# Kernel optimization log

Hardware: AMD Instinct MI355X
Metric: run time of the kernel (lower is better)

The kernel has to match this reference:

```python
import jax, jax.numpy as jnp
import numpy as np

N_NODES = 50000
N_EDGES = 800000
IN_CH = 128
DIM = 128
OUT_CH = 2
NUM_GRAPHS = 128
BN_EPS = 1e-5


def _linear_params(key, fan_in, fan_out):
    k1, k2 = jax.random.split(key)
    bound = 1.0 / np.sqrt(fan_in)
    w = jax.random.uniform(k1, (fan_in, fan_out), jnp.float32, -bound, bound)
    b = jax.random.uniform(k2, (fan_out,), jnp.float32, -bound, bound)
    return w, b


def setup_inputs() -> dict:
    key = jax.random.key(0)
    ks = jax.random.split(key, 10)
    x = jax.random.normal(ks[0], (N_NODES, IN_CH), jnp.float32)
    edge_index = jax.random.randint(ks[1], (2, N_EDGES), 0, N_NODES, jnp.int64)
    batch = jnp.sort(jax.random.randint(ks[2], (N_NODES,), 0, NUM_GRAPHS, jnp.int64))
    w1_1, b1_1 = _linear_params(ks[3], IN_CH, DIM)
    w1_2, b1_2 = _linear_params(ks[4], DIM, DIM)
    w2_1, b2_1 = _linear_params(ks[5], DIM, DIM)
    w2_2, b2_2 = _linear_params(ks[6], DIM, DIM)
    lin1_w, lin1_b = _linear_params(ks[7], DIM, DIM)
    lin2_w, lin2_b = _linear_params(ks[8], DIM, OUT_CH)
    bnk = jax.random.split(ks[9], 2)
    return {
        'x': x, 'edge_index': edge_index, 'batch': batch,
        'w1_1': w1_1, 'b1_1': b1_1,
        'bn1_g': jax.random.normal(bnk[0], (DIM,), jnp.float32) * 0.1 + 1.0,
        'bn1_b': jnp.zeros((DIM,), jnp.float32),
        'bn1_m': jnp.zeros((DIM,), jnp.float32),
        'bn1_v': jnp.ones((DIM,), jnp.float32),
        'w1_2': w1_2, 'b1_2': b1_2,
        'w2_1': w2_1, 'b2_1': b2_1,
        'bn2_g': jax.random.normal(bnk[1], (DIM,), jnp.float32) * 0.1 + 1.0,
        'bn2_b': jnp.zeros((DIM,), jnp.float32),
        'bn2_m': jnp.zeros((DIM,), jnp.float32),
        'bn2_v': jnp.ones((DIM,), jnp.float32),
        'w2_2': w2_2, 'b2_2': b2_2,
        'lin1_w': lin1_w, 'lin1_b': lin1_b,
        'lin2_w': lin2_w, 'lin2_b': lin2_b,
    }


def _bn_eval(h, g, b, m, v):
    return (h - m) * jax.lax.rsqrt(v + BN_EPS) * g + b


def _gin_conv(x, src, dst, w_a, b_a, bn_g, bn_b, bn_m, bn_v, w_b, b_b):
    # GINConv, eps=0: h = MLP(x + sum_{j->i} x_j)
    agg = jax.ops.segment_sum(x[src], dst, num_segments=x.shape[0])
    h = x + agg
    h = jax.nn.relu(_bn_eval(h @ w_a + b_a, bn_g, bn_b, bn_m, bn_v))
    return jax.nn.relu(h @ w_b + b_b)


def reference(x, edge_index, batch,
              w1_1, b1_1, bn1_g, bn1_b, bn1_m, bn1_v, w1_2, b1_2,
              w2_1, b2_1, bn2_g, bn2_b, bn2_m, bn2_v, w2_2, b2_2,
              lin1_w, lin1_b, lin2_w, lin2_b):
    src, dst = edge_index[0], edge_index[1]
    h = _gin_conv(x, src, dst, w1_1, b1_1, bn1_g, bn1_b, bn1_m, bn1_v, w1_2, b1_2)
    h = _gin_conv(h, src, dst, w2_1, b2_1, bn2_g, bn2_b, bn2_m, bn2_v, w2_2, b2_2)
    # global_add_pool over graph ids
    g = jax.ops.segment_sum(h, batch, num_segments=NUM_GRAPHS)
    g = jax.nn.relu(g @ lin1_w + lin1_b)
    # dropout is identity in eval mode
    return g @ lin2_w + lin2_b
```

## Files before the change

kernel.cpp:

```cpp
#include <hip/hip_runtime.h>
#include <hip/hip_bf16.h>

#define N_NODES 50000
#define N_EDGES 800000
#define DIM 128
#define NUM_GRAPHS 128
#define BN_EPS 1e-5f

constexpr int BK     = 7;
constexpr int NBUCK  = (N_NODES + 127) >> BK;
constexpr int TILE   = 4096;
constexpr int NTILE  = (N_EDGES + TILE - 1) / TILE;
constexpr int CAP    = 4096;
constexpr int NPAD   = N_NODES;

constexpr int XGRID  = 6250;
constexpr int WGRID  = 256;

typedef __attribute__((ext_vector_type(8))) short short8;
typedef __attribute__((ext_vector_type(4))) float f32x4;

__device__ __forceinline__ unsigned short f2bu(float v)
{
    __hip_bfloat16 h = __float2bfloat16(v);
    unsigned short u;
    __builtin_memcpy(&u, &h, 2);
    return u;
}
__device__ __forceinline__ float lo2f(unsigned int v)
{
    return __builtin_bit_cast(float, v << 16);
}
__device__ __forceinline__ float hi2f(unsigned int v)
{
    return __builtin_bit_cast(float, v & 0xffff0000u);
}
__device__ __forceinline__ float b2f(unsigned short u)
{
    return __builtin_bit_cast(float, ((unsigned int)u) << 16);
}

__global__ __launch_bounds__(256)
void setup_kernel(const float* __restrict__ x, __hip_bfloat16* __restrict__ xb,
                  const float* __restrict__ w0, const float* __restrict__ w1,
                  const float* __restrict__ w2, const float* __restrict__ w3,
                  __hip_bfloat16* __restrict__ wt, int* __restrict__ bcur,
                  float* __restrict__ G, __hip_bfloat16* __restrict__ Hb)
{
    int b = blockIdx.x;
    int t = threadIdx.x;
    if (b < XGRID) {
        size_t i = ((size_t)b * 256 + t) * 4;
        float4 v = *reinterpret_cast<const float4*>(x + i);
        uint2 o;
        o.x = (unsigned int)f2bu(v.x) | ((unsigned int)f2bu(v.y) << 16);
        o.y = (unsigned int)f2bu(v.z) | ((unsigned int)f2bu(v.w) << 16);
        *reinterpret_cast<uint2*>(reinterpret_cast<unsigned short*>(xb) + i) = o;
    } else if (b < XGRID + WGRID) {
        int o = (b - XGRID) * 256 + t;
        int m = o >> 14, idx = o & 16383;
        const float* W = (m == 0) ? w0 : (m == 1) ? w1 : (m == 2) ? w2 : w3;
        int n = idx >> 7, k = idx & 127;
        wt[o] = __float2bfloat16(W[k * 128 + n]);
    } else {
        for (int i = t; i < NBUCK; i += 256) bcur[i] = 0;
        for (int i = t; i < NUM_GRAPHS * DIM; i += 256) G[i] = 0.f;
        if (t < 128) {
            xb[(size_t)NPAD * DIM + t] = __float2bfloat16(0.f);
            Hb[(size_t)NPAD * DIM + t] = __float2bfloat16(0.f);
        }
    }
}

__global__ __launch_bounds__(512)
void bscatter_kernel(const int* __restrict__ src, const int* __restrict__ dst,
                     int* __restrict__ bcur, unsigned int* __restrict__ bedge)
{
    __shared__ int h[512];
    __shared__ int s[512];
    __shared__ int lofs[512];
    __shared__ int cur[512];
    __shared__ int gofs[512];
    __shared__ unsigned int stage[TILE];

    int t = threadIdx.x;
    h[t] = 0;
    __syncthreads();

    int e0 = blockIdx.x * TILE;
    for (int i = t; i < TILE; i += 512) {
        int e = e0 + i;
        if (e < N_EDGES) atomicAdd(&h[dst[e] >> BK], 1);
    }
    __syncthreads();

    int v = h[t];
    s[t] = v;
    __syncthreads();
    for (int o = 1; o < 512; o <<= 1) {
        int a = (t >= o) ? s[t - o] : 0;
        __syncthreads();
        s[t] += a;
        __syncthreads();
    }
    int excl = s[t] - v;
    lofs[t] = excl;
    cur[t]  = excl;
    if (t < NBUCK)
        gofs[t] = v ? atomicAdd(&bcur[t], v) : 0;
    __syncthreads();

    const int mtot = s[511];

    for (int i = t; i < TILE; i += 512) {
        int e = e0 + i;
        if (e < N_EDGES) {
            int d = dst[e];
            int b = d >> BK;
            int r = atomicAdd(&cur[b], 1);
            stage[r] = (unsigned int)src[e]
                     | ((unsigned int)(d & 127) << 16)
                     | ((unsigned int)b << 23);
        }
    }
    __syncthreads();

    for (int i = t; i < mtot; i += 512) {
        unsigned int w = stage[i];
        int b = (int)(w >> 23);
        int pos = gofs[b] + (i - lofs[b]);
        if (pos < CAP)
            bedge[(size_t)b * CAP + pos] = w & 0x7fffffu;
    }
}

__global__ __launch_bounds__(256)
void bcsr_kernel(const unsigned int* __restrict__ bedge,
                 const int* __restrict__ bcur,
                 int* __restrict__ rowbeg, int* __restrict__ rowend,
                 unsigned short* __restrict__ elist)
{
    __shared__ int h2[128];
    __shared__ int sc[128];
    __shared__ int cur[128];

    int b  = blockIdx.x;
    int t  = threadIdx.x;
    int m  = bcur[b];
    if (m > CAP) m = CAP;
    const int e0 = b * CAP;
    const unsigned int* be = bedge + (size_t)e0;

    if (t < 128) h2[t] = 0;
    __syncthreads();
    for (int i = t; i < m; i += 256)
        atomicAdd(&h2[(be[i] >> 16) & 127], 1);
    __syncthreads();

    int pc = 0;
    if (t < 128) {
        pc = (h2[t] + 15) & ~15;
        sc[t] = pc;
    }
    __syncthreads();
    for (int o = 1; o < 128; o <<= 1) {
        int a = 0;
        if (t < 128 && t >= o) a = sc[t - o];
        __syncthreads();
        if (t < 128) sc[t] += a;
        __syncthreads();
    }
    if (t < 128) {
        int ex = sc[t] - pc;
        int node = (b << BK) + t;
        if (node < N_NODES) {
            rowbeg[node] = e0 + ex;
            rowend[node] = e0 + ex + pc;
        }
        cur[t] = ex;
        int cnt = h2[t];
        for (int i = ex + cnt; i < ex + pc && i < CAP; ++i)
            elist[e0 + i] = (unsigned short)NPAD;
    }
    __syncthreads();

    for (int i = t; i < m; i += 256) {
        unsigned int w = be[i];
        int n = (int)((w >> 16) & 127);
        int r = atomicAdd(&cur[n], 1);
        if (r < CAP)
            elist[e0 + r] = (unsigned short)(w & 0xffffu);
    }
}

__device__ __forceinline__ void accum8(float* acc, uint4 v)
{
    acc[0] += lo2f(v.x); acc[1] += hi2f(v.x);
    acc[2] += lo2f(v.y); acc[3] += hi2f(v.y);
    acc[4] += lo2f(v.z); acc[5] += hi2f(v.z);
    acc[6] += lo2f(v.w); acc[7] += hi2f(v.w);
}

__global__ __launch_bounds__(256)
void gather_agg_kernel(const __hip_bfloat16* __restrict__ feat,
                       const int* __restrict__ rowbeg,
                       const int* __restrict__ rowend,
                       const unsigned short* __restrict__ elist,
                       __hip_bfloat16* __restrict__ out)
{
    const int node = blockIdx.x * 4 + (threadIdx.x >> 6);
    const int l = threadIdx.x & 63;
    const int g = l & 15;
    const int s = l >> 4;
    const uint4* F = reinterpret_cast<const uint4*>(feat);

    int p = rowbeg[node];
    const int e = rowend[node];

    float acc[8] = {};
    if (s == 0)
        accum8(acc, F[(size_t)node * 16 + g]);

    for (; p + 32 <= e; p += 32) {
        int i0 = elist[p + s];
        int i1 = elist[p + 4 + s];
        int i2 = elist[p + 8 + s];
        int i3 = elist[p + 12 + s];
        int i4 = elist[p + 16 + s];
        int i5 = elist[p + 20 + s];
        int i6 = elist[p + 24 + s];
        int i7 = elist[p + 28 + s];
        uint4 v0 = F[(size_t)i0 * 16 + g];
        uint4 v1 = F[(size_t)i1 * 16 + g];
        uint4 v2 = F[(size_t)i2 * 16 + g];
        uint4 v3 = F[(size_t)i3 * 16 + g];
        uint4 v4 = F[(size_t)i4 * 16 + g];
        uint4 v5 = F[(size_t)i5 * 16 + g];
        uint4 v6 = F[(size_t)i6 * 16 + g];
        uint4 v7 = F[(size_t)i7 * 16 + g];
        accum8(acc, v0);
        accum8(acc, v1);
        accum8(acc, v2);
        accum8(acc, v3);
        accum8(acc, v4);
        accum8(acc, v5);
        accum8(acc, v6);
        accum8(acc, v7);
    }
    if (p < e) {
        int i0 = elist[p + s];
        int i1 = elist[p + 4 + s];
        int i2 = elist[p + 8 + s];
        int i3 = elist[p + 12 + s];
        uint4 v0 = F[(size_t)i0 * 16 + g];
        uint4 v1 = F[(size_t)i1 * 16 + g];
        uint4 v2 = F[(size_t)i2 * 16 + g];
        uint4 v3 = F[(size_t)i3 * 16 + g];
        accum8(acc, v0);
        accum8(acc, v1);
        accum8(acc, v2);
        accum8(acc, v3);
    }

    #pragma unroll
    for (int j = 0; j < 8; ++j) {
        acc[j] += __shfl_xor(acc[j], 16);
        acc[j] += __shfl_xor(acc[j], 32);
    }

    if (s == 0) {
        uint4 o;
        o.x = (unsigned int)f2bu(acc[0]) | ((unsigned int)f2bu(acc[1]) << 16);
        o.y = (unsigned int)f2bu(acc[2]) | ((unsigned int)f2bu(acc[3]) << 16);
        o.z = (unsigned int)f2bu(acc[4]) | ((unsigned int)f2bu(acc[5]) << 16);
        o.w = (unsigned int)f2bu(acc[6]) | ((unsigned int)f2bu(acc[7]) << 16);
        reinterpret_cast<uint4*>(out)[(size_t)node * 16 + g] = o;
    }
}

template<int POOL>
__global__ __launch_bounds__(256)
void mlp_kernel(const __hip_bfloat16* __restrict__ A,
                const __hip_bfloat16* __restrict__ W1t,
                const __hip_bfloat16* __restrict__ W2t,
                const float* __restrict__ b1,
                const float* __restrict__ bng, const float* __restrict__ bnb,
                const float* __restrict__ bnm, const float* __restrict__ bnv,
                const float* __restrict__ b2,
                __hip_bfloat16* __restrict__ out,
                const int* __restrict__ batch, float* __restrict__ G,
                int M)
{
    __shared__ __align__(16) short sW[128 * 136];
    __shared__ __align__(16) short sT[64 * 136];

    const int t    = threadIdx.x;
    const int w    = t >> 6;
    const int l    = t & 63;
    const int lr   = l & 15;
    const int lk   = (l >> 4) << 3;
    const int orow = (l >> 4) << 2;
    const int row0b = blockIdx.x * 64;
    const int row0 = row0b + w * 16;

    const short* w1s = reinterpret_cast<const short*>(W1t);
    #pragma unroll
    for (int i = t; i < 2048; i += 256) {
        int r = i >> 4, c8 = (i & 15) << 3;
        *reinterpret_cast<short8*>(&sW[r * 136 + c8]) =
            *reinterpret_cast<const short8*>(&w1s[r * 128 + c8]);
    }

    float sc1[8], sh1[8];
    #pragma unroll
    for (int ct = 0; ct < 8; ++ct) {
        int c = ct * 16 + lr;
        float s = bng[c] * rsqrtf(bnv[c] + BN_EPS);
        sc1[ct] = s;
        sh1[ct] = (b1[c] - bnm[c]) * s + bnb[c];
    }

    const short* Ab = reinterpret_cast<const short*>(A);
    const int arow = row0 + lr;
    short8 af[4];
    #pragma unroll
    for (int ks = 0; ks < 4; ++ks) {
        short8 z = {};
        af[ks] = (arow < M)
            ? *reinterpret_cast<const short8*>(Ab + (size_t)arow * DIM + ks * 32 + lk)
            : z;
    }

    __syncthreads();

    f32x4 acc[8] = {};
    #pragma unroll
    for (int ks = 0; ks < 4; ++ks) {
        #pragma unroll
        for (int ct = 0; ct < 8; ++ct) {
            short8 bf = *reinterpret_cast<const short8*>(
                &sW[(ct * 16 + lr) * 136 + ks * 32 + lk]);
            acc[ct] = __builtin_amdgcn_mfma_f32_16x16x32_bf16(af[ks], bf, acc[ct], 0, 0, 0);
        }
    }

    #pragma unroll
    for (int ct = 0; ct < 8; ++ct) {
        #pragma unroll
        for (int q = 0; q < 4; ++q) {
            float v = fmaxf(acc[ct][q] * sc1[ct] + sh1[ct], 0.f);
            sT[(w * 16 + orow + q) * 136 + ct * 16 + lr] = (short)f2bu(v);
        }
    }

    __syncthreads();
    const short* w2s = reinterpret_cast<const short*>(W2t);
    #pragma unroll
    for (int i = t; i < 2048; i += 256) {
        int r = i >> 4, c8 = (i & 15) << 3;
        *reinterpret_cast<short8*>(&sW[r * 136 + c8]) =
            *reinterpret_cast<const short8*>(&w2s[r * 128 + c8]);
    }
    __syncthreads();

    f32x4 acc2[8] = {};
    #pragma unroll
    for (int ks = 0; ks < 4; ++ks) {
        short8 tf = *reinterpret_cast<const short8*>(
            &sT[(w * 16 + lr) * 136 + ks * 32 + lk]);
        #pragma unroll
        for (int ct = 0; ct < 8; ++ct) {
            short8 bf = *reinterpret_cast<const short8*>(
                &sW[(ct * 16 + lr) * 136 + ks * 32 + lk]);
            acc2[ct] = __builtin_amdgcn_mfma_f32_16x16x32_bf16(tf, bf, acc2[ct], 0, 0, 0);
        }
    }

    if constexpr (!POOL) {
        #pragma unroll
        for (int ct = 0; ct < 8; ++ct) {
            float bi = b2[ct * 16 + lr];
            #pragma unroll
            for (int q = 0; q < 4; ++q) {
                int r = row0 + orow + q;
                if (r < M) {
                    float v = fmaxf(acc2[ct][q] + bi, 0.f);
                    out[(size_t)r * DIM + ct * 16 + lr] = __float2bfloat16(v);
                }
            }
        }
    } else {
        #pragma unroll
        for (int ct = 0; ct < 8; ++ct) {
            float bi = b2[ct * 16 + lr];
            #pragma unroll
            for (int q = 0; q < 4; ++q) {
                float v = fmaxf(acc2[ct][q] + bi, 0.f);
                sT[(w * 16 + orow + q) * 136 + ct * 16 + lr] = (short)f2bu(v);
            }
        }
        __syncthreads();
        const int c  = t & 127;
        const int rh = t >> 7;
        float run = 0.f;
        int gcur = -1;
        for (int r = rh * 32; r < rh * 32 + 32; ++r) {
            int node = row0b + r;
            if (node >= M) break;
            int gb = batch[node];
            if (gb != gcur) {
                if (gcur >= 0 && run != 0.f) atomicAdd(&G[gcur * DIM + c], run);
                gcur = gb;
                run = 0.f;
            }
            run += b2f((unsigned short)sT[r * 136 + c]);
        }
        if (gcur >= 0 && run != 0.f) atomicAdd(&G[gcur * DIM + c], run);
    }
}

__global__ __launch_bounds__(128)
void head_kernel(const float* __restrict__ G,
                 const float* __restrict__ w1, const float* __restrict__ b1f,
                 const float* __restrict__ w2, const float* __restrict__ b2f,
                 float* __restrict__ out)
{
    __shared__ float sg[DIM];
    __shared__ float r0[DIM], r1[DIM];
    const int r = blockIdx.x;
    const int c = threadIdx.x;

    sg[c] = G[r * DIM + c];
    __syncthreads();

    float a = b1f[c];
    #pragma unroll 8
    for (int k = 0; k < DIM; ++k)
        a = fmaf(sg[k], w1[k * DIM + c], a);
    float g2 = fmaxf(a, 0.f);
    r0[c] = g2 * w2[c * 2];
    r1[c] = g2 * w2[c * 2 + 1];
    __syncthreads();

    for (int off = 64; off > 0; off >>= 1) {
        if (c < off) { r0[c] += r0[c + off]; r1[c] += r1[c + off]; }
        __syncthreads();
    }
    if (c == 0) {
        out[r * 2]     = r0[0] + b2f[0];
        out[r * 2 + 1] = r1[0] + b2f[1];
    }
}

extern "C" void kernel_launch(void* const* d_in, const int* in_sizes, int n_in,
                              void* d_out, int out_size, void* d_ws, size_t ws_size,
                              hipStream_t stream)
{
    const float* x    = (const float*)d_in[0];
    const int*   ei   = (const int*)d_in[1];
    const int*   src  = ei;
    const int*   dst  = ei + N_EDGES;
    const int*   batch= (const int*)d_in[2];
    const float* w1_1 = (const float*)d_in[3];
    const float* b1_1 = (const float*)d_in[4];
    const float* bn1g = (const float*)d_in[5];
    const float* bn1b = (const float*)d_in[6];
    const float* bn1m = (const float*)d_in[7];
    const float* bn1v = (const float*)d_in[8];
    const float* w1_2 = (const float*)d_in[9];
    const float* b1_2 = (const float*)d_in[10];
    const float* w2_1 = (const float*)d_in[11];
    const float* b2_1 = (const float*)d_in[12];
    const float* bn2g = (const float*)d_in[13];
    const float* bn2b = (const float*)d_in[14];
    const float* bn2m = (const float*)d_in[15];
    const float* bn2v = (const float*)d_in[16];
    const float* w2_2 = (const float*)d_in[17];
    const float* b2_2 = (const float*)d_in[18];
    const float* lin1w= (const float*)d_in[19];
    const float* lin1b= (const float*)d_in[20];
    const float* lin2w= (const float*)d_in[21];
    const float* lin2b= (const float*)d_in[22];

    const size_t NBE  = (size_t)N_NODES * DIM;
    const size_t NBEP = NBE + DIM;
    __hip_bfloat16* xb = (__hip_bfloat16*)d_ws;
    __hip_bfloat16* Ab = xb + NBEP;
    __hip_bfloat16* Hb = Ab + NBE;
    __hip_bfloat16* Wt = Hb + NBEP;
    float* G  = (float*)(Wt + 4 * 16384);
    int* rowbeg = (int*)(G + NUM_GRAPHS * DIM);
    int* rowend = rowbeg + N_NODES;
    int* bcur   = rowend + N_NODES;
    unsigned int* bedge = (unsigned int*)(bcur + NBUCK + 1);
    unsigned short* elist = (unsigned short*)(bedge + (size_t)NBUCK * CAP);

    const int gather_grid = N_NODES / 4;
    const int mlp_grid    = (N_NODES + 63) / 64;

    setup_kernel<<<XGRID + WGRID + 1, 256, 0, stream>>>(
        x, xb, w1_1, w1_2, w2_1, w2_2, Wt, bcur, G, Hb);
    bscatter_kernel<<<NTILE, 512, 0, stream>>>(src, dst, bcur, bedge);
    bcsr_kernel<<<NBUCK, 256, 0, stream>>>(bedge, bcur, rowbeg, rowend, elist);

    gather_agg_kernel<<<gather_grid, 256, 0, stream>>>(xb, rowbeg, rowend, elist, Ab);
    mlp_kernel<0><<<mlp_grid, 256, 0, stream>>>(
        Ab, Wt, Wt + 16384, b1_1, bn1g, bn1b, bn1m, bn1v, b1_2, Hb,
        batch, G, N_NODES);

    gather_agg_kernel<<<gather_grid, 256, 0, stream>>>(Hb, rowbeg, rowend, elist, Ab);
    mlp_kernel<1><<<mlp_grid, 256, 0, stream>>>(
        Ab, Wt + 2 * 16384, Wt + 3 * 16384, b2_1, bn2g, bn2b, bn2m, bn2v, b2_2,
        (__hip_bfloat16*)nullptr, batch, G, N_NODES);

    head_kernel<<<NUM_GRAPHS, 128, 0, stream>>>(
        G, lin1w, lin1b, lin2w, lin2b, (float*)d_out);
}
```

Before: 140.1 us.

## Merge preprocessing kernels and fuse head into MLP2 via grid barriers

Replaces the setup, bucket-scatter and CSR-build kernels with one persistent prep kernel that separates the phases with software grid barriers. The second MLP kernel becomes persistent, loops over tiles, and runs the pooled-graph head after a grid barrier, so the separate head launch goes away. The aim is to cut kernel launch and drain overhead between small dependent stages. In exchange it relies on every block being co-resident for the spin barriers, and adds a memset to reset the barrier counters.

```diff
diff --git a/kernel.cpp b/kernel.cpp
--- a/kernel.cpp
+++ b/kernel.cpp
@@ -14,8 +14,8 @@
 constexpr int CAP    = 4096;
 constexpr int NPAD   = N_NODES;
 
-constexpr int XGRID  = 6250;
-constexpr int WGRID  = 256;
+constexpr int PREP_GRID = 400;
+constexpr int MLP2_GRID = 512;
 
 typedef __attribute__((ext_vector_type(8))) short short8;
 typedef __attribute__((ext_vector_type(4))) float f32x4;
@@ -40,41 +40,30 @@
     return __builtin_bit_cast(float, ((unsigned int)u) << 16);
 }
 
-__global__ __launch_bounds__(256)
-void setup_kernel(const float* __restrict__ x, __hip_bfloat16* __restrict__ xb,
-                  const float* __restrict__ w0, const float* __restrict__ w1,
-                  const float* __restrict__ w2, const float* __restrict__ w3,
-                  __hip_bfloat16* __restrict__ wt, int* __restrict__ bcur,
-                  float* __restrict__ G, __hip_bfloat16* __restrict__ Hb)
-{
-    int b = blockIdx.x;
-    int t = threadIdx.x;
-    if (b < XGRID) {
-        size_t i = ((size_t)b * 256 + t) * 4;
-        float4 v = *reinterpret_cast<const float4*>(x + i);
-        uint2 o;
-        o.x = (unsigned int)f2bu(v.x) | ((unsigned int)f2bu(v.y) << 16);
-        o.y = (unsigned int)f2bu(v.z) | ((unsigned int)f2bu(v.w) << 16);
-        *reinterpret_cast<uint2*>(reinterpret_cast<unsigned short*>(xb) + i) = o;
-    } else if (b < XGRID + WGRID) {
-        int o = (b - XGRID) * 256 + t;
-        int m = o >> 14, idx = o & 16383;
-        const float* W = (m == 0) ? w0 : (m == 1) ? w1 : (m == 2) ? w2 : w3;
-        int n = idx >> 7, k = idx & 127;
-        wt[o] = __float2bfloat16(W[k * 128 + n]);
-    } else {
-        for (int i = t; i < NBUCK; i += 256) bcur[i] = 0;
-        for (int i = t; i < NUM_GRAPHS * DIM; i += 256) G[i] = 0.f;
-        if (t < 128) {
-            xb[(size_t)NPAD * DIM + t] = __float2bfloat16(0.f);
-            Hb[(size_t)NPAD * DIM + t] = __float2bfloat16(0.f);
-        }
-    }
-}
-
-__global__ __launch_bounds__(512)
-void bscatter_kernel(const int* __restrict__ src, const int* __restrict__ dst,
-                     int* __restrict__ bcur, unsigned int* __restrict__ bedge)
+__device__ __forceinline__ void grid_barrier(int* cnt, int target)
+{
+    __syncthreads();
+    if (threadIdx.x == 0) {
+        __threadfence();
+        atomicAdd(cnt, 1);
+        while (atomicAdd(cnt, 0) < target)
+            __builtin_amdgcn_s_sleep(8);
+        __threadfence();
+    }
+    __syncthreads();
+}
+
+__global__ __launch_bounds__(512, 4)
+void prep_kernel(const float* __restrict__ x, __hip_bfloat16* __restrict__ xb,
+                 const float* __restrict__ w0, const float* __restrict__ w1,
+                 const float* __restrict__ w2, const float* __restrict__ w3,
+                 __hip_bfloat16* __restrict__ wt, int* __restrict__ bcur,
+                 float* __restrict__ G, __hip_bfloat16* __restrict__ Hb,
+                 const int* __restrict__ src, const int* __restrict__ dst,
+                 unsigned int* __restrict__ bedge,
+                 int* __restrict__ rowbeg, int* __restrict__ rowend,
+                 unsigned short* __restrict__ elist,
+                 int* __restrict__ gcnt)
 {
     __shared__ int h[512];
     __shared__ int s[512];
@@ -83,113 +72,134 @@
     __shared__ int gofs[512];
     __shared__ unsigned int stage[TILE];
 
-    int t = threadIdx.x;
-    h[t] = 0;
-    __syncthreads();
-
-    int e0 = blockIdx.x * TILE;
-    for (int i = t; i < TILE; i += 512) {
-        int e = e0 + i;
-        if (e < N_EDGES) atomicAdd(&h[dst[e] >> BK], 1);
-    }
-    __syncthreads();
-
-    int v = h[t];
-    s[t] = v;
-    __syncthreads();
-    for (int o = 1; o < 512; o <<= 1) {
-        int a = (t >= o) ? s[t - o] : 0;
-        __syncthreads();
-        s[t] += a;
-        __syncthreads();
-    }
-    int excl = s[t] - v;
-    lofs[t] = excl;
-    cur[t]  = excl;
-    if (t < NBUCK)
-        gofs[t] = v ? atomicAdd(&bcur[t], v) : 0;
-    __syncthreads();
-
-    const int mtot = s[511];
-
-    for (int i = t; i < TILE; i += 512) {
-        int e = e0 + i;
-        if (e < N_EDGES) {
-            int d = dst[e];
-            int b = d >> BK;
-            int r = atomicAdd(&cur[b], 1);
-            stage[r] = (unsigned int)src[e]
-                     | ((unsigned int)(d & 127) << 16)
-                     | ((unsigned int)b << 23);
-        }
-    }
-    __syncthreads();
-
-    for (int i = t; i < mtot; i += 512) {
-        unsigned int w = stage[i];
-        int b = (int)(w >> 23);
-        int pos = gofs[b] + (i - lofs[b]);
-        if (pos < CAP)
-            bedge[(size_t)b * CAP + pos] = w & 0x7fffffu;
-    }
-}
-
-__global__ __launch_bounds__(256)
-void bcsr_kernel(const unsigned int* __restrict__ bedge,
-                 const int* __restrict__ bcur,
-                 int* __restrict__ rowbeg, int* __restrict__ rowend,
-                 unsigned short* __restrict__ elist)
-{
-    __shared__ int h2[128];
-    __shared__ int sc[128];
-    __shared__ int cur[128];
-
-    int b  = blockIdx.x;
-    int t  = threadIdx.x;
-    int m  = bcur[b];
-    if (m > CAP) m = CAP;
-    const int e0 = b * CAP;
-    const unsigned int* be = bedge + (size_t)e0;
-
-    if (t < 128) h2[t] = 0;
-    __syncthreads();
-    for (int i = t; i < m; i += 256)
-        atomicAdd(&h2[(be[i] >> 16) & 127], 1);
-    __syncthreads();
-
-    int pc = 0;
-    if (t < 128) {
-        pc = (h2[t] + 15) & ~15;
-        sc[t] = pc;
-    }
-    __syncthreads();
-    for (int o = 1; o < 128; o <<= 1) {
-        int a = 0;
-        if (t < 128 && t >= o) a = sc[t - o];
-        __syncthreads();
-        if (t < 128) sc[t] += a;
-        __syncthreads();
-    }
-    if (t < 128) {
-        int ex = sc[t] - pc;
-        int node = (b << BK) + t;
-        if (node < N_NODES) {
-            rowbeg[node] = e0 + ex;
-            rowend[node] = e0 + ex + pc;
-        }
-        cur[t] = ex;
-        int cnt = h2[t];
-        for (int i = ex + cnt; i < ex + pc && i < CAP; ++i)
-            elist[e0 + i] = (unsigned short)NPAD;
-    }
-    __syncthreads();
-
-    for (int i = t; i < m; i += 256) {
-        unsigned int w = be[i];
-        int n = (int)((w >> 16) & 127);
-        int r = atomicAdd(&cur[n], 1);
-        if (r < CAP)
-            elist[e0 + r] = (unsigned short)(w & 0xffffu);
+    const int t = threadIdx.x;
+    const int gtid = blockIdx.x * 512 + t;
+    const int gstride = gridDim.x * 512;
+
+    const int NQ = N_NODES * DIM / 4;
+    for (int i = gtid; i < NQ; i += gstride) {
+        size_t base = (size_t)i * 4;
+        float4 v = *reinterpret_cast<const float4*>(x + base);
+        uint2 o;
+        o.x = (unsigned int)f2bu(v.x) | ((unsigned int)f2bu(v.y) << 16);
+        o.y = (unsigned int)f2bu(v.z) | ((unsigned int)f2bu(v.w) << 16);
+        *reinterpret_cast<uint2*>(reinterpret_cast<unsigned short*>(xb) + base) = o;
+    }
+    for (int o = gtid; o < 4 * 16384; o += gstride) {
+        int m = o >> 14, idx = o & 16383;
+        const float* W = (m == 0) ? w0 : (m == 1) ? w1 : (m == 2) ? w2 : w3;
+        int n = idx >> 7, k = idx & 127;
+        wt[o] = __float2bfloat16(W[k * 128 + n]);
+    }
+    if (gtid < NBUCK) bcur[gtid] = 0;
+    if (gtid < NUM_GRAPHS * DIM) G[gtid] = 0.f;
+    if (gtid < DIM) {
+        xb[(size_t)NPAD * DIM + gtid] = __float2bfloat16(0.f);
+        Hb[(size_t)NPAD * DIM + gtid] = __float2bfloat16(0.f);
+    }
+
+    grid_barrier(gcnt, PREP_GRID);
+
+    if (blockIdx.x < NTILE) {
+        h[t] = 0;
+        __syncthreads();
+
+        int e0 = blockIdx.x * TILE;
+        for (int i = t; i < TILE; i += 512) {
+            int e = e0 + i;
+            if (e < N_EDGES) atomicAdd(&h[dst[e] >> BK], 1);
+        }
+        __syncthreads();
+
+        int v = h[t];
+        s[t] = v;
+        __syncthreads();
+        for (int o = 1; o < 512; o <<= 1) {
+            int a = (t >= o) ? s[t - o] : 0;
+            __syncthreads();
+            s[t] += a;
+            __syncthreads();
+        }
+        int excl = s[t] - v;
+        lofs[t] = excl;
+        cur[t]  = excl;
+        if (t < NBUCK)
+            gofs[t] = v ? atomicAdd(&bcur[t], v) : 0;
+        __syncthreads();
+
+        const int mtot = s[511];
+
+        for (int i = t; i < TILE; i += 512) {
+            int e = e0 + i;
+            if (e < N_EDGES) {
+                int d = dst[e];
+                int b = d >> BK;
+                int r = atomicAdd(&cur[b], 1);
+                stage[r] = (unsigned int)src[e]
+                         | ((unsigned int)(d & 127) << 16)
+                         | ((unsigned int)b << 23);
+            }
+        }
+        __syncthreads();
+
+        for (int i = t; i < mtot; i += 512) {
+            unsigned int w = stage[i];
+            int b = (int)(w >> 23);
+            int pos = gofs[b] + (i - lofs[b]);
+            if (pos < CAP)
+                bedge[(size_t)b * CAP + pos] = w & 0x7fffffu;
+        }
+    }
+
+    grid_barrier(gcnt, 2 * PREP_GRID);
+
+    if (blockIdx.x < NBUCK) {
+        const int b = blockIdx.x;
+        int m = bcur[b];
+        if (m > CAP) m = CAP;
+        const int e0 = b * CAP;
+        const unsigned int* be = bedge + (size_t)e0;
+
+        if (t < 128) h[t] = 0;
+        __syncthreads();
+        for (int i = t; i < m; i += 512)
+            atomicAdd(&h[(be[i] >> 16) & 127], 1);
+        __syncthreads();
+
+        int pc = 0;
+        if (t < 128) {
+            pc = (h[t] + 15) & ~15;
+            s[t] = pc;
+        }
+        __syncthreads();
+        for (int o = 1; o < 128; o <<= 1) {
+            int a = 0;
+            if (t < 128 && t >= o) a = s[t - o];
+            __syncthreads();
+            if (t < 128) s[t] += a;
+            __syncthreads();
+        }
+        if (t < 128) {
+            int ex = s[t] - pc;
+            int node = (b << BK) + t;
+            if (node < N_NODES) {
+                rowbeg[node] = e0 + ex;
+                rowend[node] = e0 + ex + pc;
+            }
+            cur[t] = ex;
+            int cnt = h[t];
+            for (int i = ex + cnt; i < ex + pc && i < CAP; ++i)
+                elist[e0 + i] = (unsigned short)NPAD;
+        }
+        __syncthreads();
+
+        for (int i = t; i < m; i += 512) {
+            unsigned int w = be[i];
+            int n = (int)((w >> 16) & 127);
+            int r = atomicAdd(&cur[n], 1);
+            if (r < CAP)
+                elist[e0 + r] = (unsigned short)(w & 0xffffu);
+        }
     }
 }
 
@@ -278,18 +288,15 @@
     }
 }
 
-template<int POOL>
 __global__ __launch_bounds__(256)
-void mlp_kernel(const __hip_bfloat16* __restrict__ A,
-                const __hip_bfloat16* __restrict__ W1t,
-                const __hip_bfloat16* __restrict__ W2t,
-                const float* __restrict__ b1,
-                const float* __restrict__ bng, const float* __restrict__ bnb,
-                const float* __restrict__ bnm, const float* __restrict__ bnv,
-                const float* __restrict__ b2,
-                __hip_bfloat16* __restrict__ out,
-                const int* __restrict__ batch, float* __restrict__ G,
-                int M)
+void mlp1_kernel(const __hip_bfloat16* __restrict__ A,
+                 const __hip_bfloat16* __restrict__ W1t,
+                 const __hip_bfloat16* __restrict__ W2t,
+                 const float* __restrict__ b1,
+                 const float* __restrict__ bng, const float* __restrict__ bnb,
+                 const float* __restrict__ bnm, const float* __restrict__ bnv,
+                 const float* __restrict__ b2,
+                 __hip_bfloat16* __restrict__ out, int M)
 {
     __shared__ __align__(16) short sW[128 * 136];
     __shared__ __align__(16) short sT[64 * 136];
@@ -300,8 +307,7 @@
     const int lr   = l & 15;
     const int lk   = (l >> 4) << 3;
     const int orow = (l >> 4) << 2;
-    const int row0b = blockIdx.x * 64;
-    const int row0 = row0b + w * 16;
+    const int row0 = blockIdx.x * 64 + w * 16;
 
     const short* w1s = reinterpret_cast<const short*>(W1t);
     #pragma unroll
@@ -376,26 +382,133 @@
         }
     }
 
-    if constexpr (!POOL) {
+    #pragma unroll
+    for (int ct = 0; ct < 8; ++ct) {
+        float bi = b2[ct * 16 + lr];
+        #pragma unroll
+        for (int q = 0; q < 4; ++q) {
+            int r = row0 + orow + q;
+            if (r < M) {
+                float v = fmaxf(acc2[ct][q] + bi, 0.f);
+                out[(size_t)r * DIM + ct * 16 + lr] = __float2bfloat16(v);
+            }
+        }
+    }
+}
+
+__global__ __launch_bounds__(256, 3)
+void mlp2_head_kernel(const __hip_bfloat16* __restrict__ A,
+                      const __hip_bfloat16* __restrict__ W1t,
+                      const __hip_bfloat16* __restrict__ W2t,
+                      const float* __restrict__ b1,
+                      const float* __restrict__ bng, const float* __restrict__ bnb,
+                      const float* __restrict__ bnm, const float* __restrict__ bnv,
+                      const float* __restrict__ b2,
+                      const int* __restrict__ batch, float* __restrict__ G,
+                      int M,
+                      const float* __restrict__ hw1, const float* __restrict__ hb1,
+                      const float* __restrict__ hw2, const float* __restrict__ hb2,
+                      float* __restrict__ out,
+                      int* __restrict__ gcnt)
+{
+    __shared__ __align__(16) short sW[128 * 136];
+    __shared__ __align__(16) short sT[64 * 136];
+
+    const int t    = threadIdx.x;
+    const int w    = t >> 6;
+    const int l    = t & 63;
+    const int lr   = l & 15;
+    const int lk   = (l >> 4) << 3;
+    const int orow = (l >> 4) << 2;
+    const int nt   = (M + 63) / 64;
+
+    const short* w1s = reinterpret_cast<const short*>(W1t);
+    const short* w2s = reinterpret_cast<const short*>(W2t);
+    const short* Ab  = reinterpret_cast<const short*>(A);
+
+    float sc1[8], sh1[8];
+    #pragma unroll
+    for (int ct = 0; ct < 8; ++ct) {
+        int c = ct * 16 + lr;
+        float s = bng[c] * rsqrtf(bnv[c] + BN_EPS);
+        sc1[ct] = s;
+        sh1[ct] = (b1[c] - bnm[c]) * s + bnb[c];
+    }
+    float bi2[8];
+    #pragma unroll
+    for (int ct = 0; ct < 8; ++ct) bi2[ct] = b2[ct * 16 + lr];
+
+    for (int tile = blockIdx.x; tile < nt; tile += gridDim.x) {
+        __syncthreads();
+        const int row0b = tile * 64;
+        const int row0  = row0b + w * 16;
+
+        #pragma unroll
+        for (int i = t; i < 2048; i += 256) {
+            int r = i >> 4, c8 = (i & 15) << 3;
+            *reinterpret_cast<short8*>(&sW[r * 136 + c8]) =
+                *reinterpret_cast<const short8*>(&w1s[r * 128 + c8]);
+        }
+
+        const int arow = row0 + lr;
+        short8 af[4];
+        #pragma unroll
+        for (int ks = 0; ks < 4; ++ks) {
+            short8 z = {};
+            af[ks] = (arow < M)
+                ? *reinterpret_cast<const short8*>(Ab + (size_t)arow * DIM + ks * 32 + lk)
+                : z;
+        }
+
+        __syncthreads();
+
+        f32x4 acc[8] = {};
+        #pragma unroll
+        for (int ks = 0; ks < 4; ++ks) {
+            #pragma unroll
+            for (int ct = 0; ct < 8; ++ct) {
+                short8 bf = *reinterpret_cast<const short8*>(
+                    &sW[(ct * 16 + lr) * 136 + ks * 32 + lk]);
+                acc[ct] = __builtin_amdgcn_mfma_f32_16x16x32_bf16(af[ks], bf, acc[ct], 0, 0, 0);
+            }
+        }
+
         #pragma unroll
         for (int ct = 0; ct < 8; ++ct) {
-            float bi = b2[ct * 16 + lr];
             #pragma unroll
             for (int q = 0; q < 4; ++q) {
-                int r = row0 + orow + q;
-                if (r < M) {
-                    float v = fmaxf(acc2[ct][q] + bi, 0.f);
-                    out[(size_t)r * DIM + ct * 16 + lr] = __float2bfloat16(v);
-                }
-            }
-        }
-    } else {
+                float v = fmaxf(acc[ct][q] * sc1[ct] + sh1[ct], 0.f);
+                sT[(w * 16 + orow + q) * 136 + ct * 16 + lr] = (short)f2bu(v);
+            }
+        }
+
+        __syncthreads();
+        #pragma unroll
+        for (int i = t; i < 2048; i += 256) {
+            int r = i >> 4, c8 = (i & 15) << 3;
+            *reinterpret_cast<short8*>(&sW[r * 136 + c8]) =
+                *reinterpret_cast<const short8*>(&w2s[r * 128 + c8]);
+        }
+        __syncthreads();
+
+        f32x4 acc2[8] = {};
+        #pragma unroll
+        for (int ks = 0; ks < 4; ++ks) {
+            short8 tf = *reinterpret_cast<const short8*>(
+                &sT[(w * 16 + lr) * 136 + ks * 32 + lk]);
+            #pragma unroll
+            for (int ct = 0; ct < 8; ++ct) {
+                short8 bf = *reinterpret_cast<const short8*>(
+                    &sW[(ct * 16 + lr) * 136 + ks * 32 + lk]);
+                acc2[ct] = __builtin_amdgcn_mfma_f32_16x16x32_bf16(tf, bf, acc2[ct], 0, 0, 0);
+            }
+        }
+
         #pragma unroll
         for (int ct = 0; ct < 8; ++ct) {
-            float bi = b2[ct * 16 + lr];
             #pragma unroll
             for (int q = 0; q < 4; ++q) {
-                float v = fmaxf(acc2[ct][q] + bi, 0.f);
+                float v = fmaxf(acc2[ct][q] + bi2[ct], 0.f);
                 sT[(w * 16 + orow + q) * 136 + ct * 16 + lr] = (short)f2bu(v);
             }
         }
@@ -417,38 +530,37 @@
         }
         if (gcur >= 0 && run != 0.f) atomicAdd(&G[gcur * DIM + c], run);
     }
-}
-
-__global__ __launch_bounds__(128)
-void head_kernel(const float* __restrict__ G,
-                 const float* __restrict__ w1, const float* __restrict__ b1f,
-                 const float* __restrict__ w2, const float* __restrict__ b2f,
-                 float* __restrict__ out)
-{
-    __shared__ float sg[DIM];
-    __shared__ float r0[DIM], r1[DIM];
-    const int r = blockIdx.x;
-    const int c = threadIdx.x;
-
-    sg[c] = G[r * DIM + c];
-    __syncthreads();
-
-    float a = b1f[c];
-    #pragma unroll 8
-    for (int k = 0; k < DIM; ++k)
-        a = fmaf(sg[k], w1[k * DIM + c], a);
-    float g2 = fmaxf(a, 0.f);
-    r0[c] = g2 * w2[c * 2];
-    r1[c] = g2 * w2[c * 2 + 1];
-    __syncthreads();
-
-    for (int off = 64; off > 0; off >>= 1) {
-        if (c < off) { r0[c] += r0[c + off]; r1[c] += r1[c + off]; }
-        __syncthreads();
-    }
-    if (c == 0) {
-        out[r * 2]     = r0[0] + b2f[0];
-        out[r * 2 + 1] = r1[0] + b2f[1];
+
+    grid_barrier(gcnt, MLP2_GRID);
+
+    if (blockIdx.x < NUM_GRAPHS) {
+        float* sg = reinterpret_cast<float*>(sT);
+        float* r0 = sg + DIM;
+        float* r1 = r0 + DIM;
+        const int r = blockIdx.x;
+
+        if (t < DIM) sg[t] = G[r * DIM + t];
+        __syncthreads();
+
+        if (t < DIM) {
+            float a = hb1[t];
+            #pragma unroll 8
+            for (int k = 0; k < DIM; ++k)
+                a = fmaf(sg[k], hw1[k * DIM + t], a);
+            float g2 = fmaxf(a, 0.f);
+            r0[t] = g2 * hw2[t * 2];
+            r1[t] = g2 * hw2[t * 2 + 1];
+        }
+        __syncthreads();
+
+        for (int off = 64; off > 0; off >>= 1) {
+            if (t < off) { r0[t] += r0[t + off]; r1[t] += r1[t + off]; }
+            __syncthreads();
+        }
+        if (t == 0) {
+            out[r * 2]     = r0[0] + hb2[0];
+            out[r * 2 + 1] = r1[0] + hb2[1];
+        }
     }
 }
 
@@ -492,27 +604,28 @@
     int* rowbeg = (int*)(G + NUM_GRAPHS * DIM);
     int* rowend = rowbeg + N_NODES;
     int* bcur   = rowend + N_NODES;
-    unsigned int* bedge = (unsigned int*)(bcur + NBUCK + 1);
+    int* gcnt   = bcur + NBUCK;
+    unsigned int* bedge = (unsigned int*)(gcnt + 4);
     unsigned short* elist = (unsigned short*)(bedge + (size_t)NBUCK * CAP);
 
     const int gather_grid = N_NODES / 4;
     const int mlp_grid    = (N_NODES + 63) / 64;
 
-    setup_kernel<<<XGRID + WGRID + 1, 256, 0, stream>>>(
-        x, xb, w1_1, w1_2, w2_1, w2_2, Wt, bcur, G, Hb);
-    bscatter_kernel<<<NTILE, 512, 0, stream>>>(src, dst, bcur, bedge);
-    bcsr_kernel<<<NBUCK, 256, 0, stream>>>(bedge, bcur, rowbeg, rowend, elist);
+    hipMemsetAsync(gcnt, 0, 2 * sizeof(int), stream);
+
+    prep_kernel<<<PREP_GRID, 512, 0, stream>>>(
+        x, xb, w1_1, w1_2, w2_1, w2_2, Wt, bcur, G, Hb,
+        src, dst, bedge, rowbeg, rowend, elist, gcnt);
 
     gather_agg_kernel<<<gather_grid, 256, 0, stream>>>(xb, rowbeg, rowend, elist, Ab);
-    mlp_kernel<0><<<mlp_grid, 256, 0, stream>>>(
-        Ab, Wt, Wt + 16384, b1_1, bn1g, bn1b, bn1m, bn1v, b1_2, Hb,
-        batch, G, N_NODES);
+    mlp1_kernel<<<mlp_grid, 256, 0, stream>>>(
+        Ab, Wt, Wt + 16384, b1_1, bn1g, bn1b, bn1m, bn1v, b1_2, Hb, N_NODES);
 
     gather_agg_kernel<<<gather_grid, 256, 0, stream>>>(Hb, rowbeg, rowend, elist, Ab);
-    mlp_kernel<1><<<mlp_grid, 256, 0, stream>>>(
-        Ab, Wt + 2 * 16384, Wt + 3 * 16384, b2_1, bn2g, bn2b, bn2m, bn2v, b2_2,
-        (__hip_bfloat16*)nullptr, batch, G, N_NODES);
-
-    head_kernel<<<NUM_GRAPHS, 128, 0, stream>>>(
-        G, lin1w, lin1b, lin2w, lin2b, (float*)d_out);
-}
+
+    mlp2_head_kernel<<<MLP2_GRID, 256, 0, stream>>>(
+        Ab, Wt + 2 * 16384, Wt + 3 * 16384,
+        b2_1, bn2g, bn2b, bn2m, bn2v, b2_2,
+        batch, G, N_NODES,
+        lin1w, lin1b, lin2w, lin2b, (float*)d_out, gcnt + 1);
+}
```

New measurement: 268.0 us. 91.3% more time.
